# Kernel tuning notes

Hardware: AMD Instinct MI355X
Metric: run time of the kernel (lower is better)

## Reference

```python
import math
import jax, jax.numpy as jnp
import numpy as np

B, N, D = 16, 2048, 128
MASK_VALUE = -1000000.0


def setup_inputs() -> dict:
    key = jax.random.key(0)
    k1, k2, k3, k4 = jax.random.split(key, 4)
    queries = jax.random.normal(k1, (B, N, D), dtype=jnp.float32)
    keys = jax.random.normal(k2, (B, N, D), dtype=jnp.float32)
    values = jax.random.normal(k3, (B, N, D), dtype=jnp.float32)
    valid_lens = jax.random.randint(k4, (B,), 0, N, dtype=jnp.int32)
    return {"queries": queries, "keys": keys, "values": values, "valid_lens": valid_lens}


def reference(queries, keys, values, valid_lens):
    d = queries.shape[-1]
    # [B, Nq, Nk] full score matrix, as in the original bmm
    scores = jnp.einsum("bqd,bkd->bqk", queries, keys) / math.sqrt(d)
    # Faithful to the source bug: valid_lens.dim (a method) != 1, so it is
    # flattened and scores[idx][valid_len:] = -1e6 masks QUERY ROWS >= valid_len.
    row_idx = jnp.arange(scores.shape[1])  # [Nq]
    row_mask = row_idx[None, :, None] >= valid_lens[:, None, None]  # [B, Nq, 1]
    scores = jnp.where(row_mask, MASK_VALUE, scores)
    attn = jax.nn.softmax(scores, axis=-1)
    # dropout p=0.0 -> identity
    return jnp.einsum("bqk,bkd->bqd", attn, values)
```

## Files before the change

### kernel.cpp

```cpp
#include <hip/hip_runtime.h>

#define BN 2048
#define DD 128

typedef __attribute__((ext_vector_type(8))) short bf8;
typedef __attribute__((ext_vector_type(16))) float f16v;

__device__ __forceinline__ short bf16rne(float f) {
    unsigned u = __float_as_uint(f);
    u = (u + 0x7FFFu + ((u >> 16) & 1u)) >> 16;
    return (short)u;
}

__device__ __forceinline__ unsigned pk2(float a, float b) {
    return ((unsigned)(unsigned short)bf16rne(b) << 16) | (unsigned short)bf16rne(a);
}

__device__ __forceinline__ bf8 cvt8(float4 f0, float4 f1) {
    bf8 w;
    w[0] = bf16rne(f0.x); w[1] = bf16rne(f0.y);
    w[2] = bf16rne(f0.z); w[3] = bf16rne(f0.w);
    w[4] = bf16rne(f1.x); w[5] = bf16rne(f1.y);
    w[6] = bf16rne(f1.z); w[7] = bf16rne(f1.w);
    return w;
}

__device__ __forceinline__ void dma16(const void* gsrc, void* ldst) {
    __builtin_amdgcn_global_load_lds(
        (const __attribute__((address_space(1))) void*)gsrc,
        (__attribute__((address_space(3))) void*)ldst,
        16, 0, 0);
}

__device__ __forceinline__ void dma_tile(short* lds, const short* g, int wave, int lane) {
    const char* gp = (const char*)g + wave * 8192 + lane * 16;
    char* lp = (char*)lds + wave * 8192 + lane * 16;
    #pragma unroll
    for (int c = 0; c < 8; ++c)
        dma16(gp + c * 1024, lp + c * 1024);
}

__launch_bounds__(256, 4)
__global__ void prep_kernel(const float* __restrict__ K, const float* __restrict__ V,
                            short* __restrict__ KS, short* __restrict__ VS) {
    __shared__ short tile[128 * 136];
    const int t = threadIdx.x;
    const int blk = blockIdx.x;
    const bool isK = blk < 256;
    const int bb = isK ? blk : blk - 256;
    const int b = bb >> 4, it = bb & 15;
    const float* src = (isK ? K : V) + ((size_t)b * BN + it * 128) * DD;

    #pragma unroll
    for (int i = 0; i < 8; ++i) {
        int gid = t + 256 * i;
        int r = gid >> 4, g = gid & 15;
        float4 f0 = *(const float4*)(src + r * DD + g * 8);
        float4 f1 = *(const float4*)(src + r * DD + g * 8 + 4);
        *(bf8*)&tile[r * 136 + g * 8] = cvt8(f0, f1);
    }
    __syncthreads();

    if (isK) {
        short* dst = KS + (((size_t)b * 16 + it) << 14);
        #pragma unroll
        for (int i = 0; i < 8; ++i) {
            int o = t + 256 * i;
            int g = o >> 7, r = o & 127;
            *(bf8*)&dst[o * 8] = *(const bf8*)&tile[r * 136 + g * 8];
        }
    } else {
        short* dst = VS + (((size_t)b * 16 + it) << 14);
        #pragma unroll
        for (int i = 0; i < 4; ++i) {
            int p = t + 256 * i;
            int kg = p >> 6;
            int d0 = (p & 63) * 2;
            bf8 w0, w1;
            #pragma unroll
            for (int j = 0; j < 8; ++j) {
                unsigned u = *(const unsigned*)&tile[(kg * 8 + j) * 136 + d0];
                w0[j] = (short)(u & 0xFFFF);
                w1[j] = (short)(u >> 16);
            }
            int o = kg * 128 + d0;
            *(bf8*)&dst[o * 8] = w0;
            *(bf8*)&dst[(o + 1) * 8] = w1;
        }
    }
}

__device__ __forceinline__ void build_frags(const f16v& s, float scl, float& l,
                                            bf8 af[2], int lh) {
    float pv[16];
    #pragma unroll
    for (int r = 0; r < 16; ++r) {
        pv[r] = __builtin_amdgcn_exp2f(s[r] * scl);
        l += pv[r];
    }
    unsigned P2[8];
    #pragma unroll
    for (int G = 0; G < 4; ++G) {
        P2[G * 2 + 0] = pk2(pv[4 * G + 0], pv[4 * G + 1]);
        P2[G * 2 + 1] = pk2(pv[4 * G + 2], pv[4 * G + 3]);
    }
    #pragma unroll
    for (int s2 = 0; s2 < 2; ++s2) {
        unsigned send0 = lh ? P2[4 * s2 + 0] : P2[4 * s2 + 2];
        unsigned send1 = lh ? P2[4 * s2 + 1] : P2[4 * s2 + 3];
        unsigned r0 = (unsigned)__shfl_xor((int)send0, 32, 64);
        unsigned r1 = (unsigned)__shfl_xor((int)send1, 32, 64);
        unsigned own0 = lh ? P2[4 * s2 + 2] : P2[4 * s2 + 0];
        unsigned own1 = lh ? P2[4 * s2 + 3] : P2[4 * s2 + 1];
        union { unsigned u[4]; bf8 v; } f;
        f.u[0] = lh ? r0 : own0;
        f.u[1] = lh ? r1 : own1;
        f.u[2] = lh ? own0 : r0;
        f.u[3] = lh ? own1 : r1;
        af[s2] = f.v;
    }
}

__launch_bounds__(256, 2)
__global__ void attn3(const float* __restrict__ Q,
                      const short* __restrict__ KS,
                      const short* __restrict__ VS,
                      const int* __restrict__ VL,
                      float* __restrict__ O) {
    __shared__ __align__(16) char smem[65536 + 1024];
    short* sK = (short*)smem;
    short* sV = (short*)(smem + 32768);
    float* lSh = (float*)(smem + 65536);
    float* buf4 = (float*)smem;

    const int tid  = threadIdx.x;
    const int wave = tid >> 6;
    const int lane = tid & 63;
    const int lw   = lane & 31;
    const int lh   = lane >> 5;
    const int kq   = wave;
    const int kt   = kq * 32;

    const int L  = blockIdx.x;
    const int b  = (L & 7) | (((L >> 3) & 1) << 3);
    const int qt0 = L >> 4;
    const int q0 = qt0 * 64;

    const int vlen = VL[b];
    constexpr float SCL2 = 1.4426950408889634f * 0.08838834764831845f;

    const float scl0 = (q0 + lw      >= vlen) ? 0.0f : SCL2;
    const float scl1 = (q0 + 32 + lw >= vlen) ? 0.0f : SCL2;

    const short* kbase = KS + (((size_t)b * 16) << 14);
    const short* vbase = VS + (((size_t)b * 16) << 14);

    dma_tile(sK, kbase, wave, lane);

    bf8 qfrag[2][8];
    #pragma unroll
    for (int qt = 0; qt < 2; ++qt) {
        const float* qp = Q + ((size_t)b * BN + q0 + qt * 32 + lw) * DD;
        #pragma unroll
        for (int ks = 0; ks < 8; ++ks) {
            int d0 = ks * 16 + lh * 8;
            float4 f0 = *(const float4*)(qp + d0);
            float4 f1 = *(const float4*)(qp + d0 + 4);
            qfrag[qt][ks] = cvt8(f0, f1);
        }
    }

    f16v oacc[2][4] = {};
    float l0 = 0.0f, l1 = 0.0f;

    for (int it = 0; it < 16; ++it) {
        __syncthreads();
        dma_tile(sV, vbase + ((size_t)it << 14), wave, lane);

        f16v s0 = {}, s1 = {};
        #pragma unroll
        for (int ks = 0; ks < 8; ++ks) {
            const bf8 kf = *(const bf8*)&sK[(((ks * 2 + lh) << 7) + kt + lw) * 8];
            s0 = __builtin_amdgcn_mfma_f32_32x32x16_bf16(kf, qfrag[0][ks], s0, 0, 0, 0);
            s1 = __builtin_amdgcn_mfma_f32_32x32x16_bf16(kf, qfrag[1][ks], s1, 0, 0, 0);
        }

        bf8 af0[2], af1[2];
        build_frags(s0, scl0, l0, af0, lh);
        build_frags(s1, scl1, l1, af1, lh);

        __syncthreads();
        if (it < 15)
            dma_tile(sK, kbase + ((size_t)(it + 1) << 14), wave, lane);

        #pragma unroll
        for (int s = 0; s < 2; ++s) {
            #pragma unroll
            for (int ot = 0; ot < 4; ++ot) {
                const bf8 vf = *(const bf8*)&sV[(((kq * 4 + 2 * s + lh) << 7) + ot * 32 + lw) * 8];
                oacc[0][ot] = __builtin_amdgcn_mfma_f32_32x32x16_bf16(af0[s], vf, oacc[0][ot], 0, 0, 0);
                oacc[1][ot] = __builtin_amdgcn_mfma_f32_32x32x16_bf16(af1[s], vf, oacc[1][ot], 0, 0, 0);
            }
        }
    }

    l0 += __shfl_xor(l0, 32, 64);
    l1 += __shfl_xor(l1, 32, 64);
    __syncthreads();
    if (lh == 0) {
        lSh[wave * 64 + lw] = l0;
        lSh[wave * 64 + 32 + lw] = l1;
    }

    const size_t orow0 = (size_t)b * BN + q0;
    #pragma unroll
    for (int half = 0; half < 2; ++half) {
        #pragma unroll
        for (int qt = 0; qt < 2; ++qt) {
            #pragma unroll
            for (int oi = 0; oi < 2; ++oi) {
                int ot = half * 2 + oi;
                #pragma unroll
                for (int reg = 0; reg < 16; ++reg) {
                    int row = (reg & 3) + 8 * (reg >> 2) + 4 * lh;
                    buf4[wave * 4096 + (qt * 32 + row) * 64 + oi * 32 + lw] =
                        oacc[qt][ot][reg];
                }
            }
        }
        __syncthreads();
        #pragma unroll
        for (int i = 0; i < 16; ++i) {
            int q = wave * 16 + i;
            float ltot = lSh[q] + lSh[64 + q] + lSh[128 + q] + lSh[192 + q];
            float rinv = __builtin_amdgcn_rcpf(ltot);
            float v = buf4[q * 64 + lane] + buf4[4096 + q * 64 + lane] +
                      buf4[8192 + q * 64 + lane] + buf4[12288 + q * 64 + lane];
            O[(orow0 + q) * DD + half * 64 + lane] = v * rinv;
        }
        __syncthreads();
    }
}

__launch_bounds__(256, 2)
__global__ void attn_fallback(const float* __restrict__ Q,
                              const float* __restrict__ K,
                              const float* __restrict__ V,
                              const int* __restrict__ VL,
                              float* __restrict__ O) {
    const int b = blockIdx.x >> 7;
    const int q = ((blockIdx.x & 127) * 16) + (threadIdx.x >> 4);
    const int dl = (threadIdx.x & 15) * 8;
    const int vlen = VL[b];
    const float scl = (q >= vlen) ? 0.0f : (1.4426950408889634f * 0.08838834764831845f);
    const float* qp = Q + ((size_t)b * BN + q) * DD;
    float acc[8] = {};
    float l = 0.0f;
    for (int k = 0; k < BN; ++k) {
        const float* kp = K + ((size_t)b * BN + k) * DD;
        float s = 0.0f;
        for (int d = 0; d < DD; ++d) s += qp[d] * kp[d];
        float p = __builtin_amdgcn_exp2f(s * scl);
        l += p;
        const float* vp = V + ((size_t)b * BN + k) * DD + dl;
        #pragma unroll
        for (int e = 0; e < 8; ++e) acc[e] += p * vp[e];
    }
    float* op = O + ((size_t)b * BN + q) * DD + dl;
    #pragma unroll
    for (int e = 0; e < 8; ++e) op[e] = acc[e] / l;
}

extern "C" void kernel_launch(void* const* d_in, const int* in_sizes, int n_in,
                              void* d_out, int out_size, void* d_ws, size_t ws_size,
                              hipStream_t stream) {
    const float* Q  = (const float*)d_in[0];
    const float* K  = (const float*)d_in[1];
    const float* V  = (const float*)d_in[2];
    const int*   VL = (const int*)d_in[3];
    float* O = (float*)d_out;

    const size_t need = (size_t)2 * 16 * 16 * 16384 * sizeof(short);
    if (ws_size >= need) {
        short* KS = (short*)d_ws;
        short* VS = KS + (size_t)16 * 16 * 16384;
        prep_kernel<<<512, 256, 0, stream>>>(K, V, KS, VS);
        attn3<<<512, 256, 0, stream>>>(Q, KS, VS, VL, O);
    } else {
        attn_fallback<<<2048, 256, 0, stream>>>(Q, K, V, VL, O);
    }
}
```

Measured before the change: 148.6 us.

## Load K and V MFMA fragments directly from global memory, drop LDS staging

The attention kernel no longer stages K and V tiles into shared memory with async global-to-LDS copies and barriers. Each wave now reads its bf16 K and V fragments straight from global memory, relying on L2/L1 caching of the pre-swizzled layout. This removes two barriers per iteration and cuts shared memory from 65 KB to 33 KB, which may allow more blocks per CU. The epilogue is restructured into four 32-column passes to fit the smaller buffer. In exchange, the four waves each re-read the same K tile from global/cache, and the load-ahead double buffering is lost.

```diff
diff --git a/kernel.cpp b/kernel.cpp
--- a/kernel.cpp
+++ b/kernel.cpp
@@ -23,21 +23,6 @@
     w[4] = bf16rne(f1.x); w[5] = bf16rne(f1.y);
     w[6] = bf16rne(f1.z); w[7] = bf16rne(f1.w);
     return w;
-}
-
-__device__ __forceinline__ void dma16(const void* gsrc, void* ldst) {
-    __builtin_amdgcn_global_load_lds(
-        (const __attribute__((address_space(1))) void*)gsrc,
-        (__attribute__((address_space(3))) void*)ldst,
-        16, 0, 0);
-}
-
-__device__ __forceinline__ void dma_tile(short* lds, const short* g, int wave, int lane) {
-    const char* gp = (const char*)g + wave * 8192 + lane * 16;
-    char* lp = (char*)lds + wave * 8192 + lane * 16;
-    #pragma unroll
-    for (int c = 0; c < 8; ++c)
-        dma16(gp + c * 1024, lp + c * 1024);
 }
 
 __launch_bounds__(256, 4)
@@ -122,16 +107,14 @@
 }
 
 __launch_bounds__(256, 2)
-__global__ void attn3(const float* __restrict__ Q,
+__global__ void attn7(const float* __restrict__ Q,
                       const short* __restrict__ KS,
                       const short* __restrict__ VS,
                       const int* __restrict__ VL,
                       float* __restrict__ O) {
-    __shared__ __align__(16) char smem[65536 + 1024];
-    short* sK = (short*)smem;
-    short* sV = (short*)(smem + 32768);
-    float* lSh = (float*)(smem + 65536);
-    float* buf4 = (float*)smem;
+    __shared__ __align__(16) char smem[32768 + 1024];
+    float* buf = (float*)smem;
+    float* lSh = (float*)(smem + 32768);
 
     const int tid  = threadIdx.x;
     const int wave = tid >> 6;
@@ -152,10 +135,8 @@
     const float scl0 = (q0 + lw      >= vlen) ? 0.0f : SCL2;
     const float scl1 = (q0 + 32 + lw >= vlen) ? 0.0f : SCL2;
 
-    const short* kbase = KS + (((size_t)b * 16) << 14);
-    const short* vbase = VS + (((size_t)b * 16) << 14);
-
-    dma_tile(sK, kbase, wave, lane);
+    const bf8* kbase = (const bf8*)(KS + (((size_t)b * 16) << 14));
+    const bf8* vbase = (const bf8*)(VS + (((size_t)b * 16) << 14));
 
     bf8 qfrag[2][8];
     #pragma unroll
@@ -174,69 +155,60 @@
     float l0 = 0.0f, l1 = 0.0f;
 
     for (int it = 0; it < 16; ++it) {
-        __syncthreads();
-        dma_tile(sV, vbase + ((size_t)it << 14), wave, lane);
-
+        const bf8* kg = kbase + it * 2048;
+        const bf8* vg = vbase + it * 2048;
+
+        bf8 kf[8];
+        #pragma unroll
+        for (int ks = 0; ks < 8; ++ks)
+            kf[ks] = kg[(ks * 2 + lh) * 128 + kt + lw];
         f16v s0 = {}, s1 = {};
         #pragma unroll
         for (int ks = 0; ks < 8; ++ks) {
-            const bf8 kf = *(const bf8*)&sK[(((ks * 2 + lh) << 7) + kt + lw) * 8];
-            s0 = __builtin_amdgcn_mfma_f32_32x32x16_bf16(kf, qfrag[0][ks], s0, 0, 0, 0);
-            s1 = __builtin_amdgcn_mfma_f32_32x32x16_bf16(kf, qfrag[1][ks], s1, 0, 0, 0);
+            s0 = __builtin_amdgcn_mfma_f32_32x32x16_bf16(kf[ks], qfrag[0][ks], s0, 0, 0, 0);
+            s1 = __builtin_amdgcn_mfma_f32_32x32x16_bf16(kf[ks], qfrag[1][ks], s1, 0, 0, 0);
         }
 
         bf8 af0[2], af1[2];
         build_frags(s0, scl0, l0, af0, lh);
         build_frags(s1, scl1, l1, af1, lh);
 
-        __syncthreads();
-        if (it < 15)
-            dma_tile(sK, kbase + ((size_t)(it + 1) << 14), wave, lane);
-
-        #pragma unroll
-        for (int s = 0; s < 2; ++s) {
+        #pragma unroll
+        for (int s2 = 0; s2 < 2; ++s2) {
             #pragma unroll
             for (int ot = 0; ot < 4; ++ot) {
-                const bf8 vf = *(const bf8*)&sV[(((kq * 4 + 2 * s + lh) << 7) + ot * 32 + lw) * 8];
-                oacc[0][ot] = __builtin_amdgcn_mfma_f32_32x32x16_bf16(af0[s], vf, oacc[0][ot], 0, 0, 0);
-                oacc[1][ot] = __builtin_amdgcn_mfma_f32_32x32x16_bf16(af1[s], vf, oacc[1][ot], 0, 0, 0);
+                const bf8 vf = vg[(kq * 4 + 2 * s2 + lh) * 128 + ot * 32 + lw];
+                oacc[0][ot] = __builtin_amdgcn_mfma_f32_32x32x16_bf16(af0[s2], vf, oacc[0][ot], 0, 0, 0);
+                oacc[1][ot] = __builtin_amdgcn_mfma_f32_32x32x16_bf16(af1[s2], vf, oacc[1][ot], 0, 0, 0);
             }
         }
     }
 
     l0 += __shfl_xor(l0, 32, 64);
     l1 += __shfl_xor(l1, 32, 64);
-    __syncthreads();
     if (lh == 0) {
         lSh[wave * 64 + lw] = l0;
         lSh[wave * 64 + 32 + lw] = l1;
     }
-
     const size_t orow0 = (size_t)b * BN + q0;
     #pragma unroll
-    for (int half = 0; half < 2; ++half) {
+    for (int ot = 0; ot < 4; ++ot) {
         #pragma unroll
         for (int qt = 0; qt < 2; ++qt) {
             #pragma unroll
-            for (int oi = 0; oi < 2; ++oi) {
-                int ot = half * 2 + oi;
-                #pragma unroll
-                for (int reg = 0; reg < 16; ++reg) {
-                    int row = (reg & 3) + 8 * (reg >> 2) + 4 * lh;
-                    buf4[wave * 4096 + (qt * 32 + row) * 64 + oi * 32 + lw] =
-                        oacc[qt][ot][reg];
-                }
+            for (int reg = 0; reg < 16; ++reg) {
+                int row = (reg & 3) + 8 * (reg >> 2) + 4 * lh;
+                buf[wave * 2048 + (qt * 32 + row) * 32 + lw] = oacc[qt][ot][reg];
             }
         }
         __syncthreads();
         #pragma unroll
-        for (int i = 0; i < 16; ++i) {
-            int q = wave * 16 + i;
+        for (int i = 0; i < 8; ++i) {
+            int idx = tid + 256 * i;
+            int q = idx >> 5;
             float ltot = lSh[q] + lSh[64 + q] + lSh[128 + q] + lSh[192 + q];
-            float rinv = __builtin_amdgcn_rcpf(ltot);
-            float v = buf4[q * 64 + lane] + buf4[4096 + q * 64 + lane] +
-                      buf4[8192 + q * 64 + lane] + buf4[12288 + q * 64 + lane];
-            O[(orow0 + q) * DD + half * 64 + lane] = v * rinv;
+            float v = buf[idx] + buf[2048 + idx] + buf[4096 + idx] + buf[6144 + idx];
+            O[(orow0 + q) * DD + ot * 32 + (idx & 31)] = v * __builtin_amdgcn_rcpf(ltot);
         }
         __syncthreads();
     }
@@ -280,12 +252,13 @@
     const int*   VL = (const int*)d_in[3];
     float* O = (float*)d_out;
 
-    const size_t need = (size_t)2 * 16 * 16 * 16384 * sizeof(short);
+    const size_t ks_elems = (size_t)16 * 16 * 16384;
+    const size_t need = 2 * ks_elems * sizeof(short);
     if (ws_size >= need) {
         short* KS = (short*)d_ws;
-        short* VS = KS + (size_t)16 * 16 * 16384;
+        short* VS = KS + ks_elems;
         prep_kernel<<<512, 256, 0, stream>>>(K, V, KS, VS);
-        attn3<<<512, 256, 0, stream>>>(Q, KS, VS, VL, O);
+        attn7<<<512, 256, 0, stream>>>(Q, KS, VS, VL, O);
     } else {
         attn_fallback<<<2048, 256, 0, stream>>>(Q, K, V, VL, O);
     }
```

Measured after the change: 179.2 us. +20.6%, slower.
